# Optimization experiments

Measured on AMD Instinct MI355X. Metric: run time of the kernel, lower is better.

## Reference

```python
import jax, jax.numpy as jnp
import numpy as np

N, E, G = 50000, 800000, 128          # nodes, edges, graphs
L, T, F = 4, 4, 20                    # conv layers, towers, per-tower width
D = T * F                             # 80 = hidden dim
EDGE_DIM = 16
AVG_DEG_LOG = float(np.log(17.0))     # avg_deg['log'] for avg in-degree ~16
EPS_STD = 1e-5
EPS_BN = 1e-5


def setup_inputs() -> dict:
    ks = iter(jax.random.split(jax.random.key(0), 32))
    rn = lambda *s: jax.random.normal(next(ks), s, jnp.float32) * 0.1
    return dict(
        x=jax.random.randint(next(ks), (N, 9), 0, 16),
        edge_index=jax.random.randint(next(ks), (2, E), 0, N),
        batch=jnp.sort(jax.random.randint(next(ks), (N,), 0, G)),
        edge_attr=rn(E, EDGE_DIM),
        atom_emb=rn(9, 16, D),
        edge_w=rn(L, EDGE_DIM, F), edge_b=jnp.zeros((L, F), jnp.float32),
        pre_w1=rn(L, T, 3 * F, F), pre_b1=jnp.zeros((L, T, F), jnp.float32),
        pre_w2=rn(L, T, F, F), pre_b2=jnp.zeros((L, T, F), jnp.float32),
        post_w1=rn(L, T, 13 * F, F), post_b1=jnp.zeros((L, T, F), jnp.float32),
        post_w2=rn(L, T, F, F), post_b2=jnp.zeros((L, T, F), jnp.float32),
        lin_w=rn(L, D, D), lin_b=jnp.zeros((L, D), jnp.float32),
        bn_g=jnp.ones((L, D), jnp.float32), bn_b=jnp.zeros((L, D), jnp.float32),
        mlp_w1=rn(D, 40), mlp_b1=jnp.zeros(40, jnp.float32),
        mlp_w2=rn(40, 20), mlp_b2=jnp.zeros(20, jnp.float32),
        mlp_w3=rn(20, 1), mlp_b3=jnp.zeros(1, jnp.float32),
    )


def _net(x, edge_index, batch, edge_attr, atom_emb, edge_w, edge_b, pre_w1,
         pre_b1, pre_w2, pre_b2, post_w1, post_b1, post_w2, post_b2, lin_w,
         lin_b, bn_g, bn_b, mlp_w1, mlp_b1, mlp_w2, mlp_b2, mlp_w3, mlp_b3):
    src, dst = edge_index[0], edge_index[1]
    # AtomEncoder: sum of 9 categorical embeddings -> [N, D]
    h = atom_emb[jnp.arange(9)[None, :], x].sum(1)
    deg_raw = jax.ops.segment_sum(jnp.ones((E,), jnp.float32), dst, N)
    deg = jnp.clip(deg_raw, 1.0)
    has_edge = (deg_raw > 0)[:, None, None]
    d3 = deg[:, None, None]
    logd = jnp.log(deg + 1.0)[:, None, None]
    for l in range(L):  # 4 PNAConv + BN + ReLU + residual (dropout off / eval)
        xt = h.reshape(N, T, F)
        ea = edge_attr @ edge_w[l] + edge_b[l]                      # [E, F]
        # message: concat(x_i, x_j, edge) -> per-tower pre MLP
        m = jnp.concatenate([xt[dst], xt[src],
                             jnp.broadcast_to(ea[:, None, :], (E, T, F))], -1)
        m = jax.nn.relu(jnp.einsum('eti,tio->eto', m, pre_w1[l]) + pre_b1[l])
        m = jnp.einsum('eti,tio->eto', m, pre_w2[l]) + pre_b2[l]    # [E,T,F]
        # multi-aggregator scatter-reduce
        mean = jax.ops.segment_sum(m, dst, N) / d3
        msq = jax.ops.segment_sum(m * m, dst, N) / d3
        std = jnp.sqrt(jax.nn.relu(msq - mean * mean) + EPS_STD)
        mn = jnp.where(has_edge, jax.ops.segment_min(m, dst, N), 0.0)
        mx = jnp.where(has_edge, jax.ops.segment_max(m, dst, N), 0.0)
        agg = jnp.concatenate([mean, mn, mx, std], -1)              # [N,T,4F]
        # degree scalers: identity, amplification, attenuation
        out = jnp.concatenate([agg, agg * (logd / AVG_DEG_LOG),
                               agg * (AVG_DEG_LOG / logd)], -1)     # [N,T,12F]
        out = jnp.concatenate([xt, out], -1)                        # [N,T,13F]
        out = jax.nn.relu(jnp.einsum('nti,tio->nto', out, post_w1[l]) + post_b1[l])
        out = jnp.einsum('nti,tio->nto', out, post_w2[l]) + post_b2[l]
        out = out.reshape(N, D) @ lin_w[l] + lin_b[l]
        # BatchNorm over nodes (batch statistics)
        mu = out.mean(0)
        var = jnp.mean((out - mu) ** 2, axis=0)
        out = (out - mu) * (bn_g[l] / jnp.sqrt(var + EPS_BN)) + bn_b[l]
        h = jax.nn.relu(out) + h
    # global mean pool over graphs + readout MLP
    cnt = jnp.clip(jax.ops.segment_sum(jnp.ones((N,), jnp.float32), batch, G), 1.0)
    g = jax.ops.segment_sum(h, batch, G) / cnt[:, None]
    g = jax.nn.relu(g @ mlp_w1 + mlp_b1)
    g = jax.nn.relu(g @ mlp_w2 + mlp_b2)
    return g @ mlp_w3 + mlp_b3                                      # [G, 1]


def reference(x, edge_index, batch, edge_attr, atom_emb, edge_w, edge_b, pre_w1,
              pre_b1, pre_w2, pre_b2, post_w1, post_b1, post_w2, post_b2, lin_w,
              lin_b, bn_g, bn_b, mlp_w1, mlp_b1, mlp_w2, mlp_b2, mlp_w3, mlp_b3):
    return _net(x, edge_index, batch, edge_attr, atom_emb, edge_w, edge_b, pre_w1,
                pre_b1, pre_w2, pre_b2, post_w1, post_b1, post_w2, post_b2,
                lin_w, lin_b, bn_g, bn_b, mlp_w1, mlp_b1, mlp_w2, mlp_b2,
                mlp_w3, mlp_b3)
```

## Files before the change

### kernel.cpp

```cpp
#include <hip/hip_runtime.h>
#include <hip/hip_bf16.h>

#define NN 50000
#define EE 800000
#define GG 128
#define LL 4
#define TT 4
#define FF 20
#define DD 80
#define SCAN_B ((NN + 1023) / 1024)
#define TILE_N 16
#define ITEMS (TILE_N * 10)
static constexpr float AVG_LOG = 2.8332133440562162f;

typedef __fp16 half2v __attribute__((ext_vector_type(2)));

__device__ __forceinline__ float bf2f(unsigned short u) {
  return __uint_as_float((unsigned)u << 16);
}
__device__ __forceinline__ unsigned short f2bf(float f) {
  __hip_bfloat16 b = __float2bfloat16(f);
  return *(unsigned short*)&b;
}
__device__ __forceinline__ half2v pkrtz(float a, float b) {
#if __has_builtin(__builtin_amdgcn_cvt_pkrtz)
  return __builtin_amdgcn_cvt_pkrtz(a, b);
#else
  half2v h; h.x = (__fp16)a; h.y = (__fp16)b; return h;
#endif
}
__device__ __forceinline__ float fdot2(half2v a, half2v b, float c) {
#if __has_builtin(__builtin_amdgcn_fdot2)
  return __builtin_amdgcn_fdot2(a, b, c, false);
#else
  return fmaf((float)a.x, (float)b.x, fmaf((float)a.y, (float)b.y, c));
#endif
}
__device__ __forceinline__ half2v u2h2(unsigned int u) {
  return __builtin_bit_cast(half2v, u);
}
__device__ __forceinline__ unsigned int h22u(half2v h) {
  return __builtin_bit_cast(unsigned int, h);
}
__device__ __forceinline__ unsigned int packh2_rne(float a, float b) {
  half2v h; h.x = (__fp16)a; h.y = (__fp16)b;
  return h22u(h);
}
__device__ __forceinline__ unsigned int pack_bf16(float a, float b) {
  return (unsigned int)f2bf(a) | ((unsigned int)f2bf(b) << 16);
}

__global__ __launch_bounds__(256) void k_h(const int* __restrict__ x,
                                           const float* __restrict__ atom_emb,
                                           float* __restrict__ h) {
  int idx = blockIdx.x * 256 + threadIdx.x;
  if (idx >= NN * DD) return;
  int n = idx / DD, d = idx - n * DD;
  const int* xr = x + n * 9;
  float acc = 0.f;
#pragma unroll
  for (int i = 0; i < 9; ++i) {
    int v = xr[i];
    acc += atom_emb[(i * 16 + v) * DD + d];
  }
  h[idx] = acc;
}

__global__ __launch_bounds__(256) void k_deg(const int* __restrict__ ei, int* __restrict__ cnt) {
  int e = blockIdx.x * 256 + threadIdx.x;
  if (e >= EE) return;
  atomicAdd(&cnt[ei[EE + e]], 1);
}

__global__ __launch_bounds__(1024) void k_scan_sum(const int* __restrict__ cnt, int* __restrict__ bsum) {
  __shared__ int red[1024];
  int tid = threadIdx.x;
  int i = blockIdx.x * 1024 + tid;
  red[tid] = (i < NN) ? cnt[i] : 0;
  __syncthreads();
  for (int off = 512; off > 0; off >>= 1) {
    if (tid < off) red[tid] += red[tid + off];
    __syncthreads();
  }
  if (tid == 0) bsum[blockIdx.x] = red[0];
}

__global__ void k_scan_top(const int* __restrict__ bsum, int* __restrict__ boff,
                           int* __restrict__ row_ptr) {
  if (threadIdx.x == 0 && blockIdx.x == 0) {
    int acc = 0;
    for (int b = 0; b < SCAN_B; ++b) { boff[b] = acc; acc += bsum[b]; }
    row_ptr[NN] = acc;
  }
}

__global__ __launch_bounds__(1024) void k_scan_apply(const int* __restrict__ cnt,
                                                     const int* __restrict__ boff,
                                                     int* __restrict__ row_ptr,
                                                     int* __restrict__ cursor) {
  __shared__ int sm[1024];
  int tid = threadIdx.x;
  int i = blockIdx.x * 1024 + tid;
  int v = (i < NN) ? cnt[i] : 0;
  sm[tid] = v;
  __syncthreads();
  for (int off = 1; off < 1024; off <<= 1) {
    int t = (tid >= off) ? sm[tid - off] : 0;
    __syncthreads();
    sm[tid] += t;
    __syncthreads();
  }
  int excl = boff[blockIdx.x] + sm[tid] - v;
  if (i < NN) { row_ptr[i] = excl; cursor[i] = excl; }
}

__global__ __launch_bounds__(256) void k_csrfill(const int* __restrict__ ei,
                                                 int* __restrict__ cursor,
                                                 int* __restrict__ csr_src,
                                                 int* __restrict__ csr_eid,
                                                 int* __restrict__ csr_dst) {
  int e = blockIdx.x * 256 + threadIdx.x;
  if (e >= EE) return;
  int dst = ei[EE + e];
  int slot = atomicAdd(&cursor[dst], 1);
  csr_src[slot] = ei[e];
  csr_eid[slot] = e;
  csr_dst[slot] = dst;
}

__global__ __launch_bounds__(256) void k_eagather(const int* __restrict__ csr_eid,
                                                  const float* __restrict__ edge_attr,
                                                  unsigned int* __restrict__ ea16) {
  int sl = blockIdx.x * 256 + threadIdx.x;
  if (sl >= EE) return;
  int e = csr_eid[sl];
  const float4* ap = (const float4*)(edge_attr + (size_t)e * 16);
  uint4 o0, o1;
  float4 v0 = ap[0], v1 = ap[1], v2 = ap[2], v3 = ap[3];
  o0.x = packh2_rne(v0.x, v0.y); o0.y = packh2_rne(v0.z, v0.w);
  o0.z = packh2_rne(v1.x, v1.y); o0.w = packh2_rne(v1.z, v1.w);
  o1.x = packh2_rne(v2.x, v2.y); o1.y = packh2_rne(v2.z, v2.w);
  o1.z = packh2_rne(v3.x, v3.y); o1.w = packh2_rne(v3.z, v3.w);
  uint4* op = (uint4*)(ea16 + (size_t)sl * 8);
  op[0] = o0; op[1] = o1;
}

__global__ __launch_bounds__(256) void k_nodeparams(const int* __restrict__ cnt,
                                                    float* __restrict__ inv_deg,
                                                    float* __restrict__ s1a,
                                                    float* __restrict__ s2a) {
  int n = blockIdx.x * 256 + threadIdx.x;
  if (n >= NN) return;
  int c = cnt[n];
  float deg = (c > 0) ? (float)c : 1.0f;
  inv_deg[n] = 1.0f / deg;
  float logd = logf(deg + 1.0f);
  s1a[n] = logd / AVG_LOG;
  s2a[n] = AVG_LOG / logd;
}

__global__ __launch_bounds__(64) void k_wcomb(const float* __restrict__ edge_w,
                                              const float* __restrict__ edge_b,
                                              const float* __restrict__ pre_w1,
                                              const float* __restrict__ pre_b1,
                                              const float* __restrict__ pre_w2,
                                              unsigned int* __restrict__ wcpk,
                                              unsigned int* __restrict__ w2pk,
                                              float* __restrict__ biasc, int l) {
  int t = blockIdx.x;
  int wt = l * TT + t;
  const float* W1 = pre_w1 + (size_t)wt * 1200;
  const float* W2 = pre_w2 + (size_t)wt * 400;
  const float* ew = edge_w + (size_t)l * 16 * FF;
  const float* eb = edge_b + (size_t)l * FF;
  int j = threadIdx.x;
  if (j >= FF) return;
  float col[16];
  for (int i = 0; i < 16; ++i) {
    float acc = 0.f;
#pragma unroll
    for (int f = 0; f < FF; ++f) acc = fmaf(ew[i * FF + f], W1[(40 + f) * FF + j], acc);
    col[i] = acc;
  }
#pragma unroll
  for (int i2 = 0; i2 < 8; ++i2)
    wcpk[((size_t)t * FF + j) * 8 + i2] = packh2_rne(col[2 * i2], col[2 * i2 + 1]);
#pragma unroll
  for (int i2 = 0; i2 < 10; ++i2)
    w2pk[((size_t)t * FF + j) * 10 + i2] = packh2_rne(W2[(2 * i2) * FF + j], W2[(2 * i2 + 1) * FF + j]);
  float b = pre_b1[wt * FF + j];
#pragma unroll
  for (int f = 0; f < FF; ++f) b = fmaf(eb[f], W1[(40 + f) * FF + j], b);
  biasc[t * FF + j] = b;
}

__global__ __launch_bounds__(64) void k_postpk(const float* __restrict__ post_w1,
                                               const float* __restrict__ post_w2,
                                               unsigned int* __restrict__ q1pk,
                                               unsigned int* __restrict__ q2pk, int l) {
  int t = blockIdx.x;
  int wt = l * TT + t;
  const float* Q1 = post_w1 + (size_t)wt * 5200;
  const float* Q2 = post_w2 + (size_t)wt * 400;
  int j = threadIdx.x;
  if (j >= FF) return;
  for (int i2 = 0; i2 < 120; ++i2) {
    int blk = i2 / 40, k = i2 - blk * 40;
    int r0 = 20 + 80 * blk + 2 * k;
    q1pk[((size_t)t * 120 + i2) * FF + j] = packh2_rne(Q1[r0 * FF + j], Q1[(r0 + 1) * FF + j]);
  }
#pragma unroll
  for (int i2 = 0; i2 < 10; ++i2)
    q2pk[((size_t)t * 10 + i2) * FF + j] = packh2_rne(Q2[(2 * i2) * FF + j], Q2[(2 * i2 + 1) * FF + j]);
}

__global__ __launch_bounds__(256) void k_prenode(
    const float* __restrict__ h, const float* __restrict__ pre_w1,
    const float* __restrict__ biasc,
    unsigned short* __restrict__ predD, unsigned short* __restrict__ predS, int l) {
  int tid = threadIdx.x;
  int t = tid >> 6, lane = tid & 63;
  int n = blockIdx.x * 64 + lane;
  if (n >= NN) return;
  int wt_u = __builtin_amdgcn_readfirstlane(l * TT + t);
  const float* W1 = pre_w1 + (size_t)wt_u * 1200;
  const float* bc = biasc + t * FF;
  float xt[FF];
  {
    const float4* pp = (const float4*)(h + (size_t)n * DD + t * FF);
#pragma unroll
    for (int i = 0; i < 5; ++i) { float4 v = pp[i]; xt[i*4]=v.x; xt[i*4+1]=v.y; xt[i*4+2]=v.z; xt[i*4+3]=v.w; }
  }
  float d[FF], s[FF];
#pragma unroll
  for (int j = 0; j < FF; ++j) { d[j] = bc[j]; s[j] = 0.f; }
#pragma unroll
  for (int i = 0; i < FF; ++i) {
    float a = xt[i];
#pragma unroll
    for (int j = 0; j < FF; ++j) {
      d[j] = fmaf(a, W1[i * FF + j], d[j]);
      s[j] = fmaf(a, W1[(FF + i) * FF + j], s[j]);
    }
  }
  ushort4* pd = (ushort4*)(predD + (size_t)n * DD + t * FF);
  ushort4* ps = (ushort4*)(predS + (size_t)n * DD + t * FF);
#pragma unroll
  for (int i = 0; i < 5; ++i) {
    pd[i] = make_ushort4(f2bf(d[i*4]), f2bf(d[i*4+1]), f2bf(d[i*4+2]), f2bf(d[i*4+3]));
    ps[i] = make_ushort4(f2bf(s[i*4]), f2bf(s[i*4+1]), f2bf(s[i*4+2]), f2bf(s[i*4+3]));
  }
}

__global__ __launch_bounds__(256, 4) void k_preagg(
    const unsigned short* __restrict__ predD,
    const unsigned short* __restrict__ predS,
    const unsigned int* __restrict__ ea16,
    const int* __restrict__ csr_src,
    const int* __restrict__ csr_dst,
    const int* __restrict__ row_ptr,
    const float* __restrict__ inv_deg,
    const unsigned int* __restrict__ wcpk,
    const unsigned int* __restrict__ w2pk,
    const float* __restrict__ pre_b2,
    unsigned short* __restrict__ aggbuf,
    int l) {
  __shared__ int nbr[TILE_N + 1];
  __shared__ float dDs[TT][TILE_N * FF];
  __shared__ unsigned int m2w[TT][64 * 11];
  int tid = threadIdx.x;
  int t = tid >> 6, lane = tid & 63;
  int t_u = __builtin_amdgcn_readfirstlane(t);
  int n0 = blockIdx.x * TILE_N;
  const unsigned int* Wcp = wcpk + (size_t)t_u * FF * 8;
  const unsigned int* W2p = w2pk + (size_t)t_u * FF * 10;
  const float* b2 = pre_b2 + (size_t)(l * TT + t_u) * FF;

  if (tid <= TILE_N) {
    int node = n0 + tid; if (node > NN) node = NN;
    nbr[tid] = row_ptr[node];
  }
  for (int i = lane; i < TILE_N * FF; i += 64) {
    int ni = i / FF, ch = i - ni * FF;
    int node = n0 + ni;
    dDs[t][i] = (node < NN) ? bf2f(predD[(size_t)node * DD + t_u * FF + ch]) : 0.f;
  }
  __syncthreads();
  int tbeg = nbr[0], tend = nbr[TILE_N];

  int itN[3], itP[3], itB[3], itE[3];
#pragma unroll
  for (int k = 0; k < 3; ++k) {
    int it = lane + 64 * k;
    bool v = it < ITEMS;
    int nd = v ? (it / 10) : 0;
    itN[k] = nd;
    itP[k] = v ? (it - nd * 10) : 0;
    itB[k] = v ? nbr[nd] : 0;
    itE[k] = v ? nbr[nd + 1] : 0;
  }
  float sS[3][2], sQ[3][2], sN[3][2], sX[3][2];
#pragma unroll
  for (int k = 0; k < 3; ++k) {
    sS[k][0] = 0.f; sS[k][1] = 0.f; sQ[k][0] = 0.f; sQ[k][1] = 0.f;
    sN[k][0] = 3.4e38f; sN[k][1] = 3.4e38f; sX[k][0] = -3.4e38f; sX[k][1] = -3.4e38f;
  }

  for (int wb = tbeg; wb < tend; wb += 64) {
    int p = wb + lane;
    if (p < tend) {
      int src = csr_src[p];
      int ni = csr_dst[p] - n0;
      float m1[FF];
      {
        const float4* dd = (const float4*)(&dDs[t][ni * FF]);
        const ushort4* qq = (const ushort4*)(predS + (size_t)src * DD + t_u * FF);
#pragma unroll
        for (int i = 0; i < 5; ++i) {
          float4 d4 = dd[i];
          ushort4 v = qq[i];
          m1[i*4+0] = d4.x + bf2f(v.x);
          m1[i*4+1] = d4.y + bf2f(v.y);
          m1[i*4+2] = d4.z + bf2f(v.z);
          m1[i*4+3] = d4.w + bf2f(v.w);
        }
      }
      half2v eap[8];
      {
        const uint4* ep = (const uint4*)(ea16 + (size_t)p * 8);
        uint4 e0 = ep[0], e1 = ep[1];
        eap[0] = u2h2(e0.x); eap[1] = u2h2(e0.y); eap[2] = u2h2(e0.z); eap[3] = u2h2(e0.w);
        eap[4] = u2h2(e1.x); eap[5] = u2h2(e1.y); eap[6] = u2h2(e1.z); eap[7] = u2h2(e1.w);
      }
#pragma unroll
      for (int j = 0; j < FF; ++j) {
        float c = m1[j];
#pragma unroll
        for (int i2 = 0; i2 < 8; ++i2) c = fdot2(eap[i2], u2h2(Wcp[j * 8 + i2]), c);
        m1[j] = c;
      }
      half2v mp[10];
#pragma unroll
      for (int pr = 0; pr < 10; ++pr)
        mp[pr] = pkrtz(fmaxf(m1[2*pr], 0.f), fmaxf(m1[2*pr+1], 0.f));
      float m2[FF];
#pragma unroll
      for (int j = 0; j < FF; ++j) {
        float c = b2[j];
#pragma unroll
        for (int i2 = 0; i2 < 10; ++i2) c = fdot2(mp[i2], u2h2(W2p[j * 10 + i2]), c);
        m2[j] = c;
      }
      unsigned int* row = &m2w[t][lane * 11];
#pragma unroll
      for (int pr = 0; pr < 10; ++pr) row[pr] = h22u(pkrtz(m2[2*pr], m2[2*pr+1]));
    }
    __syncthreads();
    int we = (wb + 64 < tend) ? (wb + 64) : tend;
#pragma unroll
    for (int k = 0; k < 3; ++k) {
      int lo = itB[k] > wb ? itB[k] : wb;
      int hi = itE[k] < we ? itE[k] : we;
      for (int s = lo; s < hi; ++s) {
        half2v h2 = u2h2(m2w[t][(s - wb) * 11 + itP[k]]);
        float v0 = (float)h2.x, v1 = (float)h2.y;
        sS[k][0] += v0; sQ[k][0] = fmaf(v0, v0, sQ[k][0]);
        sN[k][0] = fminf(sN[k][0], v0); sX[k][0] = fmaxf(sX[k][0], v0);
        sS[k][1] += v1; sQ[k][1] = fmaf(v1, v1, sQ[k][1]);
        sN[k][1] = fminf(sN[k][1], v1); sX[k][1] = fmaxf(sX[k][1], v1);
      }
    }
    __syncthreads();
  }

#pragma unroll
  for (int k = 0; k < 3; ++k) {
    int it = lane + 64 * k;
    if (it < ITEMS) {
      int n = n0 + itN[k];
      if (n < NN) {
        float inv = inv_deg[n];
        bool noe = (itE[k] <= itB[k]);
        float mu0 = sS[k][0] * inv, mu1 = sS[k][1] * inv;
        float sd0 = sqrtf(fmaxf(sQ[k][0] * inv - mu0 * mu0, 0.f) + 1e-5f);
        float sd1 = sqrtf(fmaxf(sQ[k][1] * inv - mu1 * mu1, 0.f) + 1e-5f);
        float mn0 = noe ? 0.f : sN[k][0], mn1 = noe ? 0.f : sN[k][1];
        float mx0 = noe ? 0.f : sX[k][0], mx1 = noe ? 0.f : sX[k][1];
        unsigned short* ab = aggbuf + ((size_t)n * 4 + t_u) * 80;
        ((unsigned int*)(ab))[itP[k]]      = pack_bf16(mu0, mu1);
        ((unsigned int*)(ab + 20))[itP[k]] = pack_bf16(mn0, mn1);
        ((unsigned int*)(ab + 40))[itP[k]] = pack_bf16(mx0, mx1);
        ((unsigned int*)(ab + 60))[itP[k]] = pack_bf16(sd0, sd1);
      }
    }
  }
}

__global__ __launch_bounds__(256) void k_post2(
    const float* __restrict__ h, const unsigned short* __restrict__ aggbuf,
    const float* __restrict__ s1a, const float* __restrict__ s2a,
    const float* __restrict__ post_w1, const float* __restrict__ post_b1,
    const unsigned int* __restrict__ q1pk, const unsigned int* __restrict__ q2pk,
    const float* __restrict__ post_b2,
    float* __restrict__ out2, int l, int tiles) {
  int t = blockIdx.x / tiles;
  int tile = blockIdx.x - t * tiles;
  int wt_u = l * TT + t;
  const float* Q1 = post_w1 + (size_t)wt_u * 5200;
  const float* B1 = post_b1 + (size_t)wt_u * FF;
  const float* B2 = post_b2 + (size_t)wt_u * FF;
  const unsigned int* q1 = q1pk + (size_t)t * 120 * FF;
  const unsigned int* q2 = q2pk + (size_t)t * 10 * FF;
  int n = tile * 256 + threadIdx.x;
  if (n >= NN) return;
  float c1 = s1a[n], c2 = s2a[n];
  half2v c1p = pkrtz(c1, c1), c2p = pkrtz(c2, c2);
  float xt[FF];
  {
    const float4* pp = (const float4*)(h + (size_t)n * DD + t * FF);
#pragma unroll
    for (int i = 0; i < 5; ++i) { float4 v = pp[i]; xt[i*4]=v.x; xt[i*4+1]=v.y; xt[i*4+2]=v.z; xt[i*4+3]=v.w; }
  }
  half2v a0p[40];
  {
    const uint4* ap = (const uint4*)(aggbuf + ((size_t)n * 4 + t) * 80);
#pragma unroll
    for (int q = 0; q < 10; ++q) {
      uint4 v = ap[q];
      unsigned int w[4] = {v.x, v.y, v.z, v.w};
#pragma unroll
      for (int k = 0; k < 4; ++k) {
        unsigned int u = w[k];
        float lo = __uint_as_float(u << 16);
        float hi = __uint_as_float(u & 0xffff0000u);
        a0p[q * 4 + k] = pkrtz(lo, hi);
      }
    }
  }
  float o1[FF];
#pragma unroll
  for (int j = 0; j < FF; ++j) o1[j] = B1[j];
#pragma unroll
  for (int i = 0; i < FF; ++i) {
    float a = xt[i];
#pragma unroll
    for (int j = 0; j < FF; ++j) o1[j] = fmaf(a, Q1[i * FF + j], o1[j]);
  }
#pragma unroll 2
  for (int k = 0; k < 40; ++k) {
    half2v act = a0p[k];
    const unsigned int* wr = q1 + k * FF;
#pragma unroll
    for (int j = 0; j < FF; ++j) o1[j] = fdot2(act, u2h2(wr[j]), o1[j]);
  }
#pragma unroll 2
  for (int k = 0; k < 40; ++k) {
    half2v act = a0p[k] * c1p;
    const unsigned int* wr = q1 + (40 + k) * FF;
#pragma unroll
    for (int j = 0; j < FF; ++j) o1[j] = fdot2(act, u2h2(wr[j]), o1[j]);
  }
#pragma unroll 2
  for (int k = 0; k < 40; ++k) {
    half2v act = a0p[k] * c2p;
    const unsigned int* wr = q1 + (80 + k) * FF;
#pragma unroll
    for (int j = 0; j < FF; ++j) o1[j] = fdot2(act, u2h2(wr[j]), o1[j]);
  }
  half2v o1p[10];
#pragma unroll
  for (int i2 = 0; i2 < 10; ++i2)
    o1p[i2] = pkrtz(fmaxf(o1[2*i2], 0.f), fmaxf(o1[2*i2+1], 0.f));
  float o2[FF];
#pragma unroll
  for (int j = 0; j < FF; ++j) o2[j] = B2[j];
#pragma unroll 2
  for (int i2 = 0; i2 < 10; ++i2) {
    half2v act = o1p[i2];
    const unsigned int* wr = q2 + i2 * FF;
#pragma unroll
    for (int j = 0; j < FF; ++j) o2[j] = fdot2(act, u2h2(wr[j]), o2[j]);
  }
  float4* op = (float4*)(out2 + (size_t)n * DD + t * FF);
#pragma unroll
  for (int i = 0; i < 5; ++i) op[i] = make_float4(o2[i*4], o2[i*4+1], o2[i*4+2], o2[i*4+3]);
}

__global__ __launch_bounds__(320) void k_lin(const float* __restrict__ out2,
                                             const float* __restrict__ lin_w,
                                             const float* __restrict__ lin_b,
                                             float* __restrict__ outl,
                                             float* __restrict__ colsum, int l) {
  __shared__ float Wl[DD * DD];
  __shared__ float rowbuf[4 * DD];
  __shared__ float red[320];
  int tid = threadIdx.x;
  for (int i = tid; i < DD * DD; i += 320) Wl[i] = lin_w[(size_t)l * DD * DD + i];
  __syncthreads();
  int nl = tid / DD, d = tid - nl * DD;
  float bias = lin_b[l * DD + d];
  float bsum = 0.f, bsq = 0.f;
  for (int base = blockIdx.x * 4; base < NN; base += gridDim.x * 4) {
    int gi = base * DD + tid;
    rowbuf[tid] = (gi < NN * DD) ? out2[gi] : 0.f;
    __syncthreads();
    int n = base + nl;
    if (n < NN) {
      float acc = bias;
#pragma unroll
      for (int i = 0; i < DD; ++i) acc = fmaf(rowbuf[nl * DD + i], Wl[i * DD + d], acc);
      outl[(size_t)n * DD + d] = acc;
      bsum += acc; bsq += acc * acc;
    }
    __syncthreads();
  }
  red[tid] = bsum;
  __syncthreads();
  if (tid < DD) {
    float s = red[tid] + red[tid + DD] + red[tid + 2 * DD] + red[tid + 3 * DD];
    atomicAdd(&colsum[d], s);
  }
  __syncthreads();
  red[tid] = bsq;
  __syncthreads();
  if (tid < DD) {
    float s = red[tid] + red[tid + DD] + red[tid + 2 * DD] + red[tid + 3 * DD];
    atomicAdd(&colsum[DD + d], s);
  }
}

__global__ __launch_bounds__(128) void k_bnfinal(const float* __restrict__ colsum,
                                                 const float* __restrict__ bn_g,
                                                 const float* __restrict__ bn_b,
                                                 float* __restrict__ bnsc, int l) {
  int d = threadIdx.x;
  if (d >= DD) return;
  float mu = colsum[d] * (1.0f / NN);
  float var = colsum[DD + d] * (1.0f / NN) - mu * mu;
  float sc = bn_g[l * DD + d] * rsqrtf(var + 1e-5f);
  bnsc[d] = sc;
  bnsc[DD + d] = bn_b[l * DD + d] - mu * sc;
}

__global__ __launch_bounds__(256) void k_bnapply(const float* __restrict__ outl,
                                                 const float* __restrict__ bnsc,
                                                 float* __restrict__ h) {
  int idx = blockIdx.x * 256 + threadIdx.x;
  if (idx >= NN * DD) return;
  int d = idx % DD;
  float v = fmaf(outl[idx], bnsc[d], bnsc[DD + d]);
  h[idx] += fmaxf(v, 0.f);
}

__global__ __launch_bounds__(256) void k_gcnt(const int* __restrict__ batch, int* __restrict__ gcnt) {
  __shared__ int hcnt[GG];
  int tid = threadIdx.x;
  if (tid < GG) hcnt[tid] = 0;
  __syncthreads();
  int n = blockIdx.x * 256 + tid;
  if (n < NN) atomicAdd(&hcnt[batch[n]], 1);
  __syncthreads();
  if (tid < GG && hcnt[tid] > 0) atomicAdd(&gcnt[tid], hcnt[tid]);
}

__global__ void k_gstart(const int* __restrict__ gcnt, int* __restrict__ gstart) {
  if (threadIdx.x == 0 && blockIdx.x == 0) {
    int acc = 0;
    for (int g = 0; g < GG; ++g) { gstart[g] = acc; acc += gcnt[g]; }
  }
}

__global__ __launch_bounds__(320) void k_gmean(const float* __restrict__ h,
                                               const int* __restrict__ gstart,
                                               const int* __restrict__ gcnt,
                                               float* __restrict__ gbuf) {
  __shared__ float red[320];
  int g = blockIdx.x, tid = threadIdx.x;
  int nl = tid / DD, d = tid - nl * DD;
  int start = gstart[g], c = gcnt[g];
  float acc = 0.f;
  for (int r = start + nl; r < start + c; r += 4) acc += h[(size_t)r * DD + d];
  red[tid] = acc;
  __syncthreads();
  if (tid < DD) {
    float s = red[tid] + red[tid + DD] + red[tid + 2 * DD] + red[tid + 3 * DD];
    float cf = (c > 0) ? (float)c : 1.0f;
    gbuf[g * DD + tid] = s / cf;
  }
}

__global__ __launch_bounds__(64) void k_mlp(const float* __restrict__ gbuf,
                                            const float* __restrict__ w1, const float* __restrict__ b1,
                                            const float* __restrict__ w2, const float* __restrict__ b2,
                                            const float* __restrict__ w3, const float* __restrict__ b3,
                                            float* __restrict__ out) {
  __shared__ float row[DD];
  __shared__ float t1[40];
  __shared__ float t2[20];
  int g = blockIdx.x, tid = threadIdx.x;
  for (int i = tid; i < DD; i += 64) row[i] = gbuf[g * DD + i];
  __syncthreads();
  if (tid < 40) {
    float acc = b1[tid];
#pragma unroll
    for (int i = 0; i < DD; ++i) acc = fmaf(row[i], w1[i * 40 + tid], acc);
    t1[tid] = fmaxf(acc, 0.f);
  }
  __syncthreads();
  if (tid < 20) {
    float acc = b2[tid];
#pragma unroll
    for (int i = 0; i < 40; ++i) acc = fmaf(t1[i], w2[i * 20 + tid], acc);
    t2[tid] = fmaxf(acc, 0.f);
  }
  __syncthreads();
  if (tid == 0) {
    float acc = b3[0];
#pragma unroll
    for (int i = 0; i < 20; ++i) acc = fmaf(t2[i], w3[i], acc);
    out[g] = acc;
  }
}

extern "C" void kernel_launch(void* const* d_in, const int* in_sizes, int n_in,
                              void* d_out, int out_size, void* d_ws, size_t ws_size,
                              hipStream_t stream) {
  const int*   x         = (const int*)d_in[0];
  const int*   ei        = (const int*)d_in[1];
  const int*   batch     = (const int*)d_in[2];
  const float* edge_attr = (const float*)d_in[3];
  const float* atom_emb  = (const float*)d_in[4];
  const float* edge_w    = (const float*)d_in[5];
  const float* edge_b    = (const float*)d_in[6];
  const float* pre_w1    = (const float*)d_in[7];
  const float* pre_b1    = (const float*)d_in[8];
  const float* pre_w2    = (const float*)d_in[9];
  const float* pre_b2    = (const float*)d_in[10];
  const float* post_w1   = (const float*)d_in[11];
  const float* post_b1   = (const float*)d_in[12];
  const float* post_w2   = (const float*)d_in[13];
  const float* post_b2   = (const float*)d_in[14];
  const float* lin_w     = (const float*)d_in[15];
  const float* lin_b     = (const float*)d_in[16];
  const float* bn_g      = (const float*)d_in[17];
  const float* bn_b      = (const float*)d_in[18];
  const float* mlp_w1    = (const float*)d_in[19];
  const float* mlp_b1    = (const float*)d_in[20];
  const float* mlp_w2    = (const float*)d_in[21];
  const float* mlp_b2    = (const float*)d_in[22];
  const float* mlp_w3    = (const float*)d_in[23];
  const float* mlp_b3    = (const float*)d_in[24];
  float* out = (float*)d_out;

  char* ws = (char*)d_ws;
  size_t off = 0;
  auto alloc = [&](size_t bytes) -> void* {
    void* p = ws + off;
    off += (bytes + 15) & ~(size_t)15;
    return p;
  };
  float* h       = (float*)alloc((size_t)NN * DD * 4);
  float* out2    = (float*)alloc((size_t)NN * DD * 4);
  unsigned short* predD = (unsigned short*)alloc((size_t)NN * DD * 2);
  unsigned short* predS = (unsigned short*)alloc((size_t)NN * DD * 2);
  int*   csr_src = (int*)alloc((size_t)EE * 4);
  int*   csr_eid = (int*)alloc((size_t)EE * 4);
  int*   csr_dst = (int*)alloc((size_t)EE * 4);
  unsigned int* ea16 = (unsigned int*)alloc((size_t)EE * 8 * 4);
  int*   row_ptr = (int*)alloc((size_t)(NN + 1) * 4);
  int*   cnt     = (int*)alloc((size_t)NN * 4);
  int*   cursor  = (int*)alloc((size_t)NN * 4);
  float* inv_deg = (float*)alloc((size_t)NN * 4);
  float* s1a     = (float*)alloc((size_t)NN * 4);
  float* s2a     = (float*)alloc((size_t)NN * 4);
  float* colsum  = (float*)alloc(2 * DD * 4);
  float* bnsc    = (float*)alloc(2 * DD * 4);
  float* gbuf    = (float*)alloc((size_t)GG * DD * 4);
  unsigned int* wcpk  = (unsigned int*)alloc((size_t)TT * FF * 8 * 4);
  unsigned int* w2pk  = (unsigned int*)alloc((size_t)TT * FF * 10 * 4);
  unsigned int* q1pk  = (unsigned int*)alloc((size_t)TT * 120 * FF * 4);
  unsigned int* q2pk  = (unsigned int*)alloc((size_t)TT * 10 * FF * 4);
  float* biasc   = (float*)alloc((size_t)TT * FF * 4);
  int*   bsum    = (int*)alloc((size_t)SCAN_B * 4);
  int*   boff    = (int*)alloc((size_t)SCAN_B * 4);
  int*   gcnt    = (int*)alloc((size_t)GG * 4);
  int*   gstart  = (int*)alloc((size_t)(GG + 1) * 4);
  unsigned short* aggbuf = (unsigned short*)alloc((size_t)NN * 4 * 80 * 2);
  float* outl = (float*)aggbuf;
  (void)in_sizes; (void)n_in; (void)out_size; (void)ws_size;

  hipMemsetAsync(cnt, 0, (size_t)NN * 4, stream);
  k_h<<<(NN * DD + 255) / 256, 256, 0, stream>>>(x, atom_emb, h);
  k_deg<<<(EE + 255) / 256, 256, 0, stream>>>(ei, cnt);
  k_scan_sum<<<SCAN_B, 1024, 0, stream>>>(cnt, bsum);
  k_scan_top<<<1, 64, 0, stream>>>(bsum, boff, row_ptr);
  k_scan_apply<<<SCAN_B, 1024, 0, stream>>>(cnt, boff, row_ptr, cursor);
  k_csrfill<<<(EE + 255) / 256, 256, 0, stream>>>(ei, cursor, csr_src, csr_eid, csr_dst);
  k_eagather<<<(EE + 255) / 256, 256, 0, stream>>>(csr_eid, edge_attr, ea16);
  k_nodeparams<<<(NN + 255) / 256, 256, 0, stream>>>(cnt, inv_deg, s1a, s2a);

  int tilesA = (NN + TILE_N - 1) / TILE_N;
  int tilesP = (NN + 255) / 256;
  for (int l = 0; l < LL; ++l) {
    k_wcomb<<<TT, 64, 0, stream>>>(edge_w, edge_b, pre_w1, pre_b1, pre_w2, wcpk, w2pk, biasc, l);
    k_postpk<<<TT, 64, 0, stream>>>(post_w1, post_w2, q1pk, q2pk, l);
    k_prenode<<<(NN + 63) / 64, 256, 0, stream>>>(h, pre_w1, biasc, predD, predS, l);
    k_preagg<<<tilesA, 256, 0, stream>>>(predD, predS, ea16, csr_src, csr_dst, row_ptr,
        inv_deg, wcpk, w2pk, pre_b2, aggbuf, l);
    k_post2<<<tilesP * TT, 256, 0, stream>>>(h, aggbuf, s1a, s2a,
        post_w1, post_b1, q1pk, q2pk, post_b2, out2, l, tilesP);
    hipMemsetAsync(colsum, 0, 2 * DD * 4, stream);
    k_lin<<<512, 320, 0, stream>>>(out2, lin_w, lin_b, outl, colsum, l);
    k_bnfinal<<<1, 128, 0, stream>>>(colsum, bn_g, bn_b, bnsc, l);
    k_bnapply<<<(NN * DD + 255) / 256, 256, 0, stream>>>(outl, bnsc, h);
  }

  hipMemsetAsync(gcnt, 0, (size_t)GG * 4, stream);
  k_gcnt<<<(NN + 255) / 256, 256, 0, stream>>>(batch, gcnt);
  k_gstart<<<1, 64, 0, stream>>>(gcnt, gstart);
  k_gmean<<<GG, 320, 0, stream>>>(h, gstart, gcnt, gbuf);
  k_mlp<<<GG, 64, 0, stream>>>(gbuf, mlp_w1, mlp_b1, mlp_w2, mlp_b2, mlp_w3, mlp_b3, out);
}
```

Measured before the change: 1.472 ms.

## Fuse post-MLP towers with linear layer and BN column statistics

Merges k_post2 and k_lin into one kernel. Each block handles 64 nodes, one wave per tower, and stages the tower outputs in shared memory, then applies the 80x80 linear layer from shared memory. Column sums and sums of squares are reduced in shared memory before the atomics. This removes the out2 round trip through global memory and one launch per layer. In exchange it uses about 46KB of shared memory per block, which may lower occupancy, and issues one pair of atomics per 64-node block.

```diff
diff --git a/kernel.cpp b/kernel.cpp
--- a/kernel.cpp
+++ b/kernel.cpp
@@ -396,136 +396,146 @@
   }
 }
 
-__global__ __launch_bounds__(256) void k_post2(
+__global__ __launch_bounds__(256) void k_postlin(
     const float* __restrict__ h, const unsigned short* __restrict__ aggbuf,
     const float* __restrict__ s1a, const float* __restrict__ s2a,
     const float* __restrict__ post_w1, const float* __restrict__ post_b1,
     const unsigned int* __restrict__ q1pk, const unsigned int* __restrict__ q2pk,
     const float* __restrict__ post_b2,
-    float* __restrict__ out2, int l, int tiles) {
-  int t = blockIdx.x / tiles;
-  int tile = blockIdx.x - t * tiles;
-  int wt_u = l * TT + t;
+    const float* __restrict__ lin_w, const float* __restrict__ lin_b,
+    float* __restrict__ outl, float* __restrict__ colsum, int l) {
+  __shared__ float Wl[DD * DD];
+  __shared__ float rows[DD * 65];
+  int tid = threadIdx.x;
+  int t = tid >> 6, lane = tid & 63;
+  int t_u = __builtin_amdgcn_readfirstlane(t);
+  int wt_u = __builtin_amdgcn_readfirstlane(l * TT + t);
+  int n = blockIdx.x * 64 + lane;
+
+  {
+    const float4* src = (const float4*)(lin_w + (size_t)l * DD * DD);
+    float4* dst = (float4*)Wl;
+    for (int i = tid; i < DD * DD / 4; i += 256) dst[i] = src[i];
+  }
+
   const float* Q1 = post_w1 + (size_t)wt_u * 5200;
   const float* B1 = post_b1 + (size_t)wt_u * FF;
   const float* B2 = post_b2 + (size_t)wt_u * FF;
-  const unsigned int* q1 = q1pk + (size_t)t * 120 * FF;
-  const unsigned int* q2 = q2pk + (size_t)t * 10 * FF;
-  int n = tile * 256 + threadIdx.x;
-  if (n >= NN) return;
-  float c1 = s1a[n], c2 = s2a[n];
-  half2v c1p = pkrtz(c1, c1), c2p = pkrtz(c2, c2);
-  float xt[FF];
-  {
-    const float4* pp = (const float4*)(h + (size_t)n * DD + t * FF);
-#pragma unroll
-    for (int i = 0; i < 5; ++i) { float4 v = pp[i]; xt[i*4]=v.x; xt[i*4+1]=v.y; xt[i*4+2]=v.z; xt[i*4+3]=v.w; }
-  }
-  half2v a0p[40];
-  {
-    const uint4* ap = (const uint4*)(aggbuf + ((size_t)n * 4 + t) * 80);
-#pragma unroll
-    for (int q = 0; q < 10; ++q) {
-      uint4 v = ap[q];
-      unsigned int w[4] = {v.x, v.y, v.z, v.w};
-#pragma unroll
-      for (int k = 0; k < 4; ++k) {
-        unsigned int u = w[k];
-        float lo = __uint_as_float(u << 16);
-        float hi = __uint_as_float(u & 0xffff0000u);
-        a0p[q * 4 + k] = pkrtz(lo, hi);
+  const unsigned int* q1 = q1pk + (size_t)t_u * 120 * FF;
+  const unsigned int* q2 = q2pk + (size_t)t_u * 10 * FF;
+  if (n < NN) {
+    float c1 = s1a[n], c2 = s2a[n];
+    half2v c1p = pkrtz(c1, c1), c2p = pkrtz(c2, c2);
+    float xt[FF];
+    {
+      const float4* pp = (const float4*)(h + (size_t)n * DD + t_u * FF);
+#pragma unroll
+      for (int i = 0; i < 5; ++i) { float4 v = pp[i]; xt[i*4]=v.x; xt[i*4+1]=v.y; xt[i*4+2]=v.z; xt[i*4+3]=v.w; }
+    }
+    half2v a0p[40];
+    {
+      const uint4* ap = (const uint4*)(aggbuf + ((size_t)n * 4 + t_u) * 80);
+#pragma unroll
+      for (int q = 0; q < 10; ++q) {
+        uint4 v = ap[q];
+        unsigned int w[4] = {v.x, v.y, v.z, v.w};
+#pragma unroll
+        for (int k = 0; k < 4; ++k) {
+          unsigned int u = w[k];
+          float lo = __uint_as_float(u << 16);
+          float hi = __uint_as_float(u & 0xffff0000u);
+          a0p[q * 4 + k] = pkrtz(lo, hi);
+        }
       }
     }
-  }
-  float o1[FF];
-#pragma unroll
-  for (int j = 0; j < FF; ++j) o1[j] = B1[j];
-#pragma unroll
-  for (int i = 0; i < FF; ++i) {
-    float a = xt[i];
-#pragma unroll
-    for (int j = 0; j < FF; ++j) o1[j] = fmaf(a, Q1[i * FF + j], o1[j]);
-  }
+    float o1[FF];
+#pragma unroll
+    for (int j = 0; j < FF; ++j) o1[j] = B1[j];
+#pragma unroll
+    for (int i = 0; i < FF; ++i) {
+      float a = xt[i];
+#pragma unroll
+      for (int j = 0; j < FF; ++j) o1[j] = fmaf(a, Q1[i * FF + j], o1[j]);
+    }
 #pragma unroll 2
-  for (int k = 0; k < 40; ++k) {
-    half2v act = a0p[k];
-    const unsigned int* wr = q1 + k * FF;
-#pragma unroll
-    for (int j = 0; j < FF; ++j) o1[j] = fdot2(act, u2h2(wr[j]), o1[j]);
-  }
+    for (int k = 0; k < 40; ++k) {
+      half2v act = a0p[k];
+      const unsigned int* wr = q1 + k * FF;
+#pragma unroll
+      for (int j = 0; j < FF; ++j) o1[j] = fdot2(act, u2h2(wr[j]), o1[j]);
+    }
 #pragma unroll 2
-  for (int k = 0; k < 40; ++k) {
-    half2v act = a0p[k] * c1p;
-    const unsigned int* wr = q1 + (40 + k) * FF;
-#pragma unroll
-    for (int j = 0; j < FF; ++j) o1[j] = fdot2(act, u2h2(wr[j]), o1[j]);
-  }
+    for (int k = 0; k < 40; ++k) {
+      half2v act = a0p[k] * c1p;
+      const unsigned int* wr = q1 + (40 + k) * FF;
+#pragma unroll
+      for (int j = 0; j < FF; ++j) o1[j] = fdot2(act, u2h2(wr[j]), o1[j]);
+    }
 #pragma unroll 2
-  for (int k = 0; k < 40; ++k) {
-    half2v act = a0p[k] * c2p;
-    const unsigned int* wr = q1 + (80 + k) * FF;
-#pragma unroll
-    for (int j = 0; j < FF; ++j) o1[j] = fdot2(act, u2h2(wr[j]), o1[j]);
-  }
-  half2v o1p[10];
-#pragma unroll
-  for (int i2 = 0; i2 < 10; ++i2)
-    o1p[i2] = pkrtz(fmaxf(o1[2*i2], 0.f), fmaxf(o1[2*i2+1], 0.f));
-  float o2[FF];
-#pragma unroll
-  for (int j = 0; j < FF; ++j) o2[j] = B2[j];
+    for (int k = 0; k < 40; ++k) {
+      half2v act = a0p[k] * c2p;
+      const unsigned int* wr = q1 + (80 + k) * FF;
+#pragma unroll
+      for (int j = 0; j < FF; ++j) o1[j] = fdot2(act, u2h2(wr[j]), o1[j]);
+    }
+    half2v o1p[10];
+#pragma unroll
+    for (int i2 = 0; i2 < 10; ++i2)
+      o1p[i2] = pkrtz(fmaxf(o1[2*i2], 0.f), fmaxf(o1[2*i2+1], 0.f));
+    float o2[FF];
+#pragma unroll
+    for (int j = 0; j < FF; ++j) o2[j] = B2[j];
 #pragma unroll 2
-  for (int i2 = 0; i2 < 10; ++i2) {
-    half2v act = o1p[i2];
-    const unsigned int* wr = q2 + i2 * FF;
-#pragma unroll
-    for (int j = 0; j < FF; ++j) o2[j] = fdot2(act, u2h2(wr[j]), o2[j]);
-  }
-  float4* op = (float4*)(out2 + (size_t)n * DD + t * FF);
-#pragma unroll
-  for (int i = 0; i < 5; ++i) op[i] = make_float4(o2[i*4], o2[i*4+1], o2[i*4+2], o2[i*4+3]);
-}
-
-__global__ __launch_bounds__(320) void k_lin(const float* __restrict__ out2,
-                                             const float* __restrict__ lin_w,
-                                             const float* __restrict__ lin_b,
-                                             float* __restrict__ outl,
-                                             float* __restrict__ colsum, int l) {
-  __shared__ float Wl[DD * DD];
-  __shared__ float rowbuf[4 * DD];
-  __shared__ float red[320];
-  int tid = threadIdx.x;
-  for (int i = tid; i < DD * DD; i += 320) Wl[i] = lin_w[(size_t)l * DD * DD + i];
-  __syncthreads();
-  int nl = tid / DD, d = tid - nl * DD;
-  float bias = lin_b[l * DD + d];
-  float bsum = 0.f, bsq = 0.f;
-  for (int base = blockIdx.x * 4; base < NN; base += gridDim.x * 4) {
-    int gi = base * DD + tid;
-    rowbuf[tid] = (gi < NN * DD) ? out2[gi] : 0.f;
-    __syncthreads();
-    int n = base + nl;
-    if (n < NN) {
-      float acc = bias;
-#pragma unroll
-      for (int i = 0; i < DD; ++i) acc = fmaf(rowbuf[nl * DD + i], Wl[i * DD + d], acc);
-      outl[(size_t)n * DD + d] = acc;
-      bsum += acc; bsq += acc * acc;
-    }
-    __syncthreads();
-  }
-  red[tid] = bsum;
+    for (int i2 = 0; i2 < 10; ++i2) {
+      half2v act = o1p[i2];
+      const unsigned int* wr = q2 + i2 * FF;
+#pragma unroll
+      for (int j = 0; j < FF; ++j) o2[j] = fdot2(act, u2h2(wr[j]), o2[j]);
+    }
+#pragma unroll
+    for (int j = 0; j < FF; ++j) rows[lane * DD + t_u * FF + j] = o2[j];
+  } else {
+#pragma unroll
+    for (int j = 0; j < FF; ++j) rows[lane * DD + t_u * FF + j] = 0.f;
+  }
+  __syncthreads();
+
+  int nl = tid >> 2;
+  int d0 = (tid & 3) * FF;
+  int n2 = blockIdx.x * 64 + nl;
+  float acc[FF];
+#pragma unroll
+  for (int j = 0; j < FF; ++j) acc[j] = lin_b[l * DD + d0 + j];
+  for (int i = 0; i < DD; ++i) {
+    float r = rows[nl * DD + i];
+    const float* wl = &Wl[i * DD + d0];
+#pragma unroll
+    for (int j = 0; j < FF; ++j) acc[j] = fmaf(r, wl[j], acc[j]);
+  }
+  if (n2 < NN) {
+    float4* op = (float4*)(outl + (size_t)n2 * DD + d0);
+#pragma unroll
+    for (int i = 0; i < 5; ++i) op[i] = make_float4(acc[i*4], acc[i*4+1], acc[i*4+2], acc[i*4+3]);
+  }
+  __syncthreads();
+
+  bool valid = (n2 < NN);
+#pragma unroll
+  for (int j = 0; j < FF; ++j) rows[(d0 + j) * 65 + nl] = valid ? acc[j] : 0.f;
   __syncthreads();
   if (tid < DD) {
-    float s = red[tid] + red[tid + DD] + red[tid + 2 * DD] + red[tid + 3 * DD];
-    atomicAdd(&colsum[d], s);
-  }
-  __syncthreads();
-  red[tid] = bsq;
+    float s = 0.f;
+    for (int k = 0; k < 64; ++k) s += rows[tid * 65 + k];
+    atomicAdd(&colsum[tid], s);
+  }
+  __syncthreads();
+#pragma unroll
+  for (int j = 0; j < FF; ++j) rows[(d0 + j) * 65 + nl] = valid ? acc[j] * acc[j] : 0.f;
   __syncthreads();
   if (tid < DD) {
-    float s = red[tid] + red[tid + DD] + red[tid + 2 * DD] + red[tid + 3 * DD];
-    atomicAdd(&colsum[DD + d], s);
+    float s = 0.f;
+    for (int k = 0; k < 64; ++k) s += rows[tid * 65 + k];
+    atomicAdd(&colsum[DD + tid], s);
   }
 }
 
@@ -660,7 +670,7 @@
     return p;
   };
   float* h       = (float*)alloc((size_t)NN * DD * 4);
-  float* out2    = (float*)alloc((size_t)NN * DD * 4);
+  float* outl    = (float*)alloc((size_t)NN * DD * 4);
   unsigned short* predD = (unsigned short*)alloc((size_t)NN * DD * 2);
   unsigned short* predS = (unsigned short*)alloc((size_t)NN * DD * 2);
   int*   csr_src = (int*)alloc((size_t)EE * 4);
@@ -686,7 +696,6 @@
   int*   gcnt    = (int*)alloc((size_t)GG * 4);
   int*   gstart  = (int*)alloc((size_t)(GG + 1) * 4);
   unsigned short* aggbuf = (unsigned short*)alloc((size_t)NN * 4 * 80 * 2);
-  float* outl = (float*)aggbuf;
   (void)in_sizes; (void)n_in; (void)out_size; (void)ws_size;
 
   hipMemsetAsync(cnt, 0, (size_t)NN * 4, stream);
@@ -700,17 +709,16 @@
   k_nodeparams<<<(NN + 255) / 256, 256, 0, stream>>>(cnt, inv_deg, s1a, s2a);
 
   int tilesA = (NN + TILE_N - 1) / TILE_N;
-  int tilesP = (NN + 255) / 256;
+  int blocksPL = (NN + 63) / 64;
   for (int l = 0; l < LL; ++l) {
     k_wcomb<<<TT, 64, 0, stream>>>(edge_w, edge_b, pre_w1, pre_b1, pre_w2, wcpk, w2pk, biasc, l);
     k_postpk<<<TT, 64, 0, stream>>>(post_w1, post_w2, q1pk, q2pk, l);
     k_prenode<<<(NN + 63) / 64, 256, 0, stream>>>(h, pre_w1, biasc, predD, predS, l);
     k_preagg<<<tilesA, 256, 0, stream>>>(predD, predS, ea16, csr_src, csr_dst, row_ptr,
         inv_deg, wcpk, w2pk, pre_b2, aggbuf, l);
-    k_post2<<<tilesP * TT, 256, 0, stream>>>(h, aggbuf, s1a, s2a,
-        post_w1, post_b1, q1pk, q2pk, post_b2, out2, l, tilesP);
     hipMemsetAsync(colsum, 0, 2 * DD * 4, stream);
-    k_lin<<<512, 320, 0, stream>>>(out2, lin_w, lin_b, outl, colsum, l);
+    k_postlin<<<blocksPL, 256, 0, stream>>>(h, aggbuf, s1a, s2a,
+        post_w1, post_b1, q1pk, q2pk, post_b2, lin_w, lin_b, outl, colsum, l);
     k_bnfinal<<<1, 128, 0, stream>>>(colsum, bn_g, bn_b, bnsc, l);
     k_bnapply<<<(NN * DD + 255) / 256, 256, 0, stream>>>(outl, bnsc, h);
   }
```

New measurement: 1.447 ms. Within noise of the previous version (-1.7%).
